# Kernel tuning notes

Hardware: AMD Instinct MI355X
Metric: run time of the kernel (lower is better)

Reference implementation:

```python
import jax, jax.numpy as jnp
import numpy as np

E = 1024
H = 16
D = E // H  # head dim 64


def setup_inputs() -> dict:
    key = jax.random.key(0)
    ks = jax.random.split(key, 6)
    s = E ** -0.5
    return {
        "x": jax.random.normal(ks[0], (2, 2048, E), dtype=jnp.float32),
        "Wq": jax.random.normal(ks[1], (E, E), dtype=jnp.float32) * s,
        "Wk": jax.random.normal(ks[2], (E, E), dtype=jnp.float32) * s,
        "Wv": jax.random.normal(ks[3], (E, E), dtype=jnp.float32) * s,
        "Wo": jax.random.normal(ks[4], (E, E), dtype=jnp.float32) * s,
        "bo": jax.random.normal(ks[5], (E,), dtype=jnp.float32) * 0.01,
    }


def reference(x, Wq, Wk, Wv, Wo, bo):
    B, T, _ = x.shape
    # per-head bias-free projections, batched as one GEMM each then split heads
    q = (x @ Wq).reshape(B, T, H, D)
    k = (x @ Wk).reshape(B, T, H, D)
    v = (x @ Wv).reshape(B, T, H, D)
    scores = jnp.einsum("bqhd,bkhd->bhqk", q, k) * (D ** -0.5)
    causal = jnp.tril(jnp.ones((T, T), dtype=bool))
    scores = jnp.where(causal, scores, -jnp.inf)
    attn = jax.nn.softmax(scores, axis=-1)  # dropout p=0 (eval)
    out = jnp.einsum("bhqk,bkhd->bqhd", attn, v).reshape(B, T, E)
    return out @ Wo + bo
```

## Files before the change

### kernel.cpp

```cpp
#include <hip/hip_runtime.h>
#include <hip/hip_bf16.h>
#include <stdint.h>

typedef __hip_bfloat16 bf16;
typedef __attribute__((ext_vector_type(8))) short bf16x8;
typedef __attribute__((ext_vector_type(4))) float f32x4;
typedef __attribute__((ext_vector_type(16))) float f32x16;

#define MFMA16(a,b,c) __builtin_amdgcn_mfma_f32_16x16x32_bf16((a),(b),(c),0,0,0)
#define MFMA32(a,b,c) __builtin_amdgcn_mfma_f32_32x32x16_bf16((a),(b),(c),0,0,0)

#define B_ 2
#define T_ 2048
#define E_ 1024
#define H_ 16
#define D_ 64
#define M_ (B_*T_)
#define PROJ_ELEMS (32ull * 2048ull * 64ull)

__device__ __forceinline__ void gload_lds16(const bf16* g, bf16* l) {
  __builtin_amdgcn_global_load_lds(
      (const __attribute__((address_space(1))) unsigned int*)g,
      (__attribute__((address_space(3))) unsigned int*)l,
      16, 0, 0);
}

__global__ __launch_bounds__(256) void cvt_x_kernel(const float* __restrict__ in,
                                                    bf16* __restrict__ out) {
  int i = blockIdx.x * 256 + threadIdx.x;
  float4 v = reinterpret_cast<const float4*>(in)[i];
  union { bf16 h[4]; unsigned long long u; } t;
  t.h[0] = __float2bfloat16(v.x);
  t.h[1] = __float2bfloat16(v.y);
  t.h[2] = __float2bfloat16(v.z);
  t.h[3] = __float2bfloat16(v.w);
  reinterpret_cast<unsigned long long*>(out)[i] = t.u;
}

__global__ __launch_bounds__(256) void transpose_cvt4_kernel(
    const float* __restrict__ W0, const float* __restrict__ W1,
    const float* __restrict__ W2, const float* __restrict__ W3,
    bf16* __restrict__ T0, bf16* __restrict__ T1,
    bf16* __restrict__ T2, bf16* __restrict__ T3) {
  __shared__ float tile[32][33];
  const float* W; bf16* Wt;
  switch (blockIdx.z) {
    case 0: W = W0; Wt = T0; break;
    case 1: W = W1; Wt = T1; break;
    case 2: W = W2; Wt = T2; break;
    default: W = W3; Wt = T3; break;
  }
  const int tx = threadIdx.x, ty = threadIdx.y;
  const int n0 = blockIdx.x * 32, k0 = blockIdx.y * 32;
#pragma unroll
  for (int i = 0; i < 4; i++)
    tile[ty + 8*i][tx] = W[(size_t)(k0 + ty + 8*i) * E_ + n0 + tx];
  __syncthreads();
#pragma unroll
  for (int i = 0; i < 4; i++)
    Wt[(size_t)(n0 + ty + 8*i) * E_ + k0 + tx] = __float2bfloat16(tile[tx][ty + 8*i]);
}

__global__ __launch_bounds__(256) void gemm_bt_kernel(
    const bf16* __restrict__ A, const bf16* __restrict__ Bt,
    void* __restrict__ out, const float* __restrict__ bias,
    const int mode, const float scale)
{
  constexpr int K = E_;
  __shared__ __align__(16) bf16 As[128*32];
  __shared__ __align__(16) bf16 Bs[128*32];
  const int tid = threadIdx.x;
  const int w = tid >> 6, l = tid & 63;
  const int lc = l & 15, lr = l >> 4;
  const int m0 = blockIdx.y * 128, n0 = blockIdx.x * 128;
  const int wr = (w >> 1) * 64, wc = (w & 1) * 64;

  f32x4 acc[4][4];
#pragma unroll
  for (int m = 0; m < 4; m++)
#pragma unroll
    for (int n = 0; n < 4; n++) acc[m][n] = (f32x4)0.0f;

  const int srow = l >> 2;
  const int scol = (l & 3) * 8;

  for (int k0 = 0; k0 < K; k0 += 32) {
#pragma unroll
    for (int p = 0; p < 2; p++) {
      const int r = (w*2 + p) * 16 + srow;
      gload_lds16(A  + (size_t)(m0 + r) * K + k0 + scol, &As[(w*2 + p) * 512]);
      gload_lds16(Bt + (size_t)(n0 + r) * K + k0 + scol, &Bs[(w*2 + p) * 512]);
    }
    __syncthreads();
    bf16x8 af[4], bfr[4];
#pragma unroll
    for (int m = 0; m < 4; m++)
      af[m] = *reinterpret_cast<const bf16x8*>(&As[(wr + m*16 + lc) * 32 + lr * 8]);
#pragma unroll
    for (int n = 0; n < 4; n++)
      bfr[n] = *reinterpret_cast<const bf16x8*>(&Bs[(wc + n*16 + lc) * 32 + lr * 8]);
#pragma unroll
    for (int m = 0; m < 4; m++)
#pragma unroll
      for (int n = 0; n < 4; n++)
        acc[m][n] = MFMA16(af[m], bfr[n], acc[m][n]);
    __syncthreads();
  }

  const int proj = blockIdx.x >> 3;
#pragma unroll
  for (int m = 0; m < 4; m++) {
#pragma unroll
    for (int n = 0; n < 4; n++) {
#pragma unroll
      for (int j = 0; j < 4; j++) {
        const int row = m0 + wr + m*16 + lr*4 + j;
        const int col = n0 + wc + n*16 + lc;
        if (mode == 2) {
          reinterpret_cast<float*>(out)[(size_t)row * E_ + col] = acc[m][n][j] + bias[col];
        } else {
          const int cp = col & (E_-1);
          const int b = row >> 11, t = row & (T_-1);
          const int h = cp >> 6,  d = cp & (D_-1);
          const float v = acc[m][n][j] * (proj == 0 ? scale : 1.0f);
          size_t idx;
          if (proj == 2) idx = (((size_t)(b*H_ + h)) * D_ + d) * T_ + t;
          else           idx = (((size_t)(b*H_ + h)) * T_ + t) * D_ + d;
          reinterpret_cast<bf16*>(out)[proj * PROJ_ELEMS + idx] = __float2bfloat16(v);
        }
      }
    }
  }
}

__global__ __launch_bounds__(256, 2) void attn_fwd_kernel(
    const bf16* __restrict__ Q, const bf16* __restrict__ Kt,
    const bf16* __restrict__ Vt, bf16* __restrict__ O)
{
  __shared__ __align__(16) bf16 Ks[2][32 * 64];
  __shared__ __align__(16) bf16 Vs[2][64 * 32];

  const int tid = threadIdx.x;
  const int w = tid >> 6, l = tid & 63;
  const int ln = l & 31;
  const int hi = l >> 5;
  const int bid = blockIdx.x;
  const int bh  = (bid & 7) * 4 + ((bid >> 3) & 3);
  const int qb  = 15 - (bid >> 5);
  const int q0  = qb * 128 + w * 32;

  const bf16* Qb = Q  + (size_t)bh * T_ * D_;
  const bf16* Kb = Kt + (size_t)bh * T_ * D_;
  const bf16* Vb = Vt + (size_t)bh * D_ * T_;

  const bf16* ksrc = Kb + (size_t)(w*8 + (l>>3)) * D_ + (((l&7) ^ (l>>3)) << 3);
  const bf16* vsrc = Vb + (size_t)(w*16 + (l>>2)) * T_ + (((l&3) ^ ((l>>2)&3)) << 3);

  bf16x8 qf[4];
#pragma unroll
  for (int s = 0; s < 4; s++)
    qf[s] = *reinterpret_cast<const bf16x8*>(
        &Qb[(size_t)(q0 + ln) * D_ + s*16 + hi*8]);

  f32x16 oacc0 = (f32x16)0.0f, oacc1 = (f32x16)0.0f;
  float mrow = -1e30f, psum = 0.0f;

  union U4 { uint32_t u[4]; bf16x8 v; };
  union PK { bf16 h[2]; uint32_t u; };

  const int my_last = 4*qb + w;
  const int nkt = 4*qb + 4;

  gload_lds16(ksrc, &Ks[0][w << 9]);
  gload_lds16(vsrc, &Vs[0][w << 9]);
  __syncthreads();

  for (int kt = 0; kt < nkt; ++kt) {
    const int buf = kt & 1;
    const int kbase = kt << 5;
    if (kt + 1 < nkt) {
      gload_lds16(ksrc + (size_t)(kbase + 32) * D_, &Ks[buf^1][w << 9]);
      gload_lds16(vsrc + (kbase + 32),              &Vs[buf^1][w << 9]);
    }
    if (kt <= my_last) {
      bf16x8 kf[4];
#pragma unroll
      for (int s = 0; s < 4; s++) {
        const int ch = 2*s + hi;
        kf[s] = *reinterpret_cast<const bf16x8*>(
            &Ks[buf][ln*64 + ((ch ^ (ln & 7)) << 3)]);
      }
      f32x16 sT = (f32x16)0.0f;
#pragma unroll
      for (int s = 0; s < 4; s++) sT = MFMA32(kf[s], qf[s], sT);

      if (kt == my_last) {
#pragma unroll
        for (int r = 0; r < 16; r++) {
          const int mm = (r&3) + 8*(r>>2) + 4*hi;
          if (mm > ln) sT[r] = -1e30f;
        }
      }

      float tmax = fmaxf(fmaxf(fmaxf(sT[0],sT[1]), fmaxf(sT[2],sT[3])),
                         fmaxf(fmaxf(sT[4],sT[5]), fmaxf(sT[6],sT[7])));
      tmax = fmaxf(tmax,
             fmaxf(fmaxf(fmaxf(sT[8],sT[9]),  fmaxf(sT[10],sT[11])),
                   fmaxf(fmaxf(sT[12],sT[13]),fmaxf(sT[14],sT[15]))));
      tmax = fmaxf(tmax, __shfl_xor(tmax, 32));
      if (!__all(tmax <= mrow + 8.0f)) {
        const float mn_ = fmaxf(mrow, tmax);
        const float fsc = exp2f(mrow - mn_);
        mrow = mn_;
        psum *= fsc;
        oacc0 *= fsc;
        oacc1 *= fsc;
      }
#pragma unroll
      for (int r = 0; r < 16; r++) {
        const float pe = exp2f(sT[r] - mrow);
        sT[r] = pe;
        psum += pe;
      }

      uint32_t u_[8];
#pragma unroll
      for (int i = 0; i < 8; i++) {
        PK pk;
        pk.h[0] = __float2bfloat16(sT[2*i]);
        pk.h[1] = __float2bfloat16(sT[2*i+1]);
        u_[i] = pk.u;
      }
      const uint32_t x0 = __shfl_xor(hi ? u_[0] : u_[2], 32);
      const uint32_t x1 = __shfl_xor(hi ? u_[1] : u_[3], 32);
      const uint32_t x2 = __shfl_xor(hi ? u_[4] : u_[6], 32);
      const uint32_t x3 = __shfl_xor(hi ? u_[5] : u_[7], 32);
      U4 pf0, pf1;
      pf0.u[0] = hi ? x0 : u_[0];  pf0.u[1] = hi ? x1 : u_[1];
      pf0.u[2] = hi ? u_[2] : x0;  pf0.u[3] = hi ? u_[3] : x1;
      pf1.u[0] = hi ? x2 : u_[4];  pf1.u[1] = hi ? x3 : u_[5];
      pf1.u[2] = hi ? u_[6] : x2;  pf1.u[3] = hi ? u_[7] : x3;

#pragma unroll
      for (int a = 0; a < 2; a++) {
        const int r0 = a*32 + ln;
        bf16x8 vf0 = *reinterpret_cast<const bf16x8*>(
            &Vs[buf][r0*32 + (((0 + hi) ^ (r0 & 3)) << 3)]);
        bf16x8 vf1 = *reinterpret_cast<const bf16x8*>(
            &Vs[buf][r0*32 + (((2 + hi) ^ (r0 & 3)) << 3)]);
        if (a == 0) {
          oacc0 = MFMA32(vf0, pf0.v, oacc0);
          oacc0 = MFMA32(vf1, pf1.v, oacc0);
        } else {
          oacc1 = MFMA32(vf0, pf0.v, oacc1);
          oacc1 = MFMA32(vf1, pf1.v, oacc1);
        }
      }
    }
    __syncthreads();
  }

  psum += __shfl_xor(psum, 32);
  const float inv = 1.0f / psum;
  const int b = bh >> 4, h = bh & 15;
  const size_t rowbase = (size_t)(b * T_ + q0 + ln) * E_ + h * 64;
#pragma unroll
  for (int r = 0; r < 16; r++) {
    const int d = (r&3) + 8*(r>>2) + 4*hi;
    O[rowbase + d] = __float2bfloat16(oacc0[r] * inv);
  }
#pragma unroll
  for (int r = 0; r < 16; r++) {
    const int d = 32 + (r&3) + 8*(r>>2) + 4*hi;
    O[rowbase + d] = __float2bfloat16(oacc1[r] * inv);
  }
}

extern "C" void kernel_launch(void* const* d_in, const int* in_sizes, int n_in,
                              void* d_out, int out_size, void* d_ws, size_t ws_size,
                              hipStream_t stream) {
  const float* x  = (const float*)d_in[0];
  const float* Wq = (const float*)d_in[1];
  const float* Wk = (const float*)d_in[2];
  const float* Wv = (const float*)d_in[3];
  const float* Wo = (const float*)d_in[4];
  const float* bo = (const float*)d_in[5];
  float* out = (float*)d_out;

  char* ws = (char*)d_ws;
  bf16* xb  = (bf16*)(ws);
  bf16* WqT = (bf16*)(ws + (8ull  << 20));
  bf16* WkT = (bf16*)(ws + (10ull << 20));
  bf16* WvT = (bf16*)(ws + (12ull << 20));
  bf16* WoT = (bf16*)(ws + (14ull << 20));
  bf16* Qb  = (bf16*)(ws + (16ull << 20));
  bf16* Ob  = (bf16*)(ws + (40ull << 20));

  cvt_x_kernel<<<4096, 256, 0, stream>>>(x, xb);
  transpose_cvt4_kernel<<<dim3(32, 32, 4), dim3(32, 8), 0, stream>>>(
      Wq, Wk, Wv, Wo, WqT, WkT, WvT, WoT);

  const float qscale = 0.125f * 1.44269504f;
  gemm_bt_kernel<<<dim3(24, 32), 256, 0, stream>>>(xb, WqT, Qb, nullptr, 3, qscale);

  attn_fwd_kernel<<<512, 256, 0, stream>>>(
      Qb, Qb + PROJ_ELEMS, Qb + 2*PROJ_ELEMS, Ob);

  gemm_bt_kernel<<<dim3(8, 32), 256, 0, stream>>>(Ob, WoT, out, bo, 2, 1.0f);
}
```

Baseline: 160.5 us.

## Deepen attention K/V LDS pipeline to four stages with vmcnt waits

Replaces the double-buffered K/V LDS staging with a 4-slot ring that prefetches three tiles ahead. Explicit s_waitcnt vmcnt plus a single barrier per iteration replace the trailing __syncthreads. The change also alters the V swizzle pattern to reduce LDS bank conflicts and raises wave priority around the MFMA blocks. Doubling LDS per block may reduce occupancy, and the hand-coded vmcnt counts must match the number of outstanding loads exactly.

```diff
diff --git a/kernel.cpp b/kernel.cpp
--- a/kernel.cpp
+++ b/kernel.cpp
@@ -137,8 +137,8 @@
     const bf16* __restrict__ Q, const bf16* __restrict__ Kt,
     const bf16* __restrict__ Vt, bf16* __restrict__ O)
 {
-  __shared__ __align__(16) bf16 Ks[2][32 * 64];
-  __shared__ __align__(16) bf16 Vs[2][64 * 32];
+  __shared__ __align__(16) bf16 Ks[4][32 * 64];
+  __shared__ __align__(16) bf16 Vs[4][64 * 32];
 
   const int tid = threadIdx.x;
   const int w = tid >> 6, l = tid & 63;
@@ -154,7 +154,7 @@
   const bf16* Vb = Vt + (size_t)bh * D_ * T_;
 
   const bf16* ksrc = Kb + (size_t)(w*8 + (l>>3)) * D_ + (((l&7) ^ (l>>3)) << 3);
-  const bf16* vsrc = Vb + (size_t)(w*16 + (l>>2)) * T_ + (((l&3) ^ ((l>>2)&3)) << 3);
+  const bf16* vsrc = Vb + (size_t)(w*16 + (l>>2)) * T_ + (((l&3) ^ ((l>>3)&3)) << 3);
 
   bf16x8 qf[4];
 #pragma unroll
@@ -171,18 +171,28 @@
   const int my_last = 4*qb + w;
   const int nkt = 4*qb + 4;
 
-  gload_lds16(ksrc, &Ks[0][w << 9]);
-  gload_lds16(vsrc, &Vs[0][w << 9]);
-  __syncthreads();
+#define STAGE(TI) do {                                                 \
+    const int rb_ = (TI) & 3;                                          \
+    gload_lds16(ksrc + (size_t)((TI) << 5) * D_, &Ks[rb_][w << 9]);    \
+    gload_lds16(vsrc + ((TI) << 5),              &Vs[rb_][w << 9]);    \
+  } while (0)
+
+  STAGE(0);
+  if (nkt > 1) STAGE(1);
+  if (nkt > 2) STAGE(2);
 
   for (int kt = 0; kt < nkt; ++kt) {
-    const int buf = kt & 1;
-    const int kbase = kt << 5;
-    if (kt + 1 < nkt) {
-      gload_lds16(ksrc + (size_t)(kbase + 32) * D_, &Ks[buf^1][w << 9]);
-      gload_lds16(vsrc + (kbase + 32),              &Vs[buf^1][w << 9]);
-    }
+    const int ahead = (nkt - kt - 1 >= 3) ? 2 : (nkt - kt - 1 >= 2 ? 1 : 0);
+    if (ahead == 2)      asm volatile("s_waitcnt vmcnt(4)" ::: "memory");
+    else if (ahead == 1) asm volatile("s_waitcnt vmcnt(2)" ::: "memory");
+    else                 asm volatile("s_waitcnt vmcnt(0)" ::: "memory");
+    __builtin_amdgcn_sched_barrier(0);
+    __builtin_amdgcn_s_barrier();
+    if (kt + 3 < nkt) STAGE(kt + 3);
+    __builtin_amdgcn_sched_barrier(0);
+
     if (kt <= my_last) {
+      const int buf = kt & 3;
       bf16x8 kf[4];
 #pragma unroll
       for (int s = 0; s < 4; s++) {
@@ -191,8 +201,10 @@
             &Ks[buf][ln*64 + ((ch ^ (ln & 7)) << 3)]);
       }
       f32x16 sT = (f32x16)0.0f;
+      __builtin_amdgcn_s_setprio(1);
 #pragma unroll
       for (int s = 0; s < 4; s++) sT = MFMA32(kf[s], qf[s], sT);
+      __builtin_amdgcn_s_setprio(0);
 
       if (kt == my_last) {
 #pragma unroll
@@ -241,13 +253,15 @@
       pf1.u[0] = hi ? x2 : u_[4];  pf1.u[1] = hi ? x3 : u_[5];
       pf1.u[2] = hi ? u_[6] : x2;  pf1.u[3] = hi ? u_[7] : x3;
 
+      __builtin_amdgcn_s_setprio(1);
 #pragma unroll
       for (int a = 0; a < 2; a++) {
         const int r0 = a*32 + ln;
+        const int sw = (r0 >> 1) & 3;
         bf16x8 vf0 = *reinterpret_cast<const bf16x8*>(
-            &Vs[buf][r0*32 + (((0 + hi) ^ (r0 & 3)) << 3)]);
+            &Vs[buf][r0*32 + (((0 + hi) ^ sw) << 3)]);
         bf16x8 vf1 = *reinterpret_cast<const bf16x8*>(
-            &Vs[buf][r0*32 + (((2 + hi) ^ (r0 & 3)) << 3)]);
+            &Vs[buf][r0*32 + (((2 + hi) ^ sw) << 3)]);
         if (a == 0) {
           oacc0 = MFMA32(vf0, pf0.v, oacc0);
           oacc0 = MFMA32(vf1, pf1.v, oacc0);
@@ -256,9 +270,10 @@
           oacc1 = MFMA32(vf1, pf1.v, oacc1);
         }
       }
+      __builtin_amdgcn_s_setprio(0);
     }
-    __syncthreads();
-  }
+  }
+#undef STAGE
 
   psum += __shfl_xor(psum, 32);
   const float inv = 1.0f / psum;
```

After: 158.4 us. No clear change (-1.3%).
